# Performance work log

Hardware: AMD Instinct MI355X
Metric: run time of the kernel (lower is better)

## Reference

```python
import jax, jax.numpy as jnp
import numpy as np


def setup_inputs() -> dict:
    key = jax.random.key(0)
    ks = jax.random.split(key, 6)
    B, N, d = 8, 2048, 64
    h = jax.random.normal(ks[0], (B, N, d), dtype=jnp.float32)
    adj = jax.random.randint(ks[1], (B, N, N), 0, 2, dtype=jnp.int32)
    h_root = jax.random.normal(ks[2], (B, N), dtype=jnp.float32)
    weight = jax.random.normal(ks[3], (d, d), dtype=jnp.float32) * (1.0 / np.sqrt(d))
    a1 = jax.random.normal(ks[4], (d, 1), dtype=jnp.float32) * (1.0 / np.sqrt(d))
    a2 = jax.random.normal(ks[5], (d, 1), dtype=jnp.float32) * (1.0 / np.sqrt(d))
    return {"h": h, "adj": adj, "h_root": h_root, "weight": weight, "a1": a1, "a2": a2}


def reference(h, adj, h_root, weight, a1, a2):
    h0 = h
    hw = jax.nn.relu(jnp.matmul(h, weight))          # (B,N,d)
    t1 = jnp.matmul(hw, a1)                          # (B,N,1)
    t2 = jnp.matmul(hw, a2)                          # (B,N,1)
    # e[b,i,j] = relu(t1[b,i] + t2[b,j])  (broadcast, same as repeat/view in torch)
    e = jax.nn.relu(t1 + jnp.swapaxes(t2, -1, -2))   # (B,N,N)
    # FAITHFUL to source bug: pos0 = -9e15 * zeros_like(adj) == 0, so
    # non-edges get logit 0 (not -inf) before softmax.
    e = jnp.where(adj > 0, e, jnp.zeros_like(e))
    attention = jax.nn.softmax(e, axis=-1)           # (B,N,N)
    embedding = jnp.matmul(attention, hw)            # (B,N,d)
    # assign = h_root[:,:,None] @ ones(B,1,d) -> h_root broadcast over d;
    # assign > 0  <=>  h_root > 0 since ones are positive.
    assign = h_root[:, :, None] * jnp.ones((1, 1, hw.shape[-1]), dtype=hw.dtype)
    embedding = jnp.where(assign > 0, embedding, h0)
    return embedding
```

## Files before the change

kernel.cpp:

```cpp
#include <hip/hip_runtime.h>
#include <hip/hip_bf16.h>

#define BATCH 8
#define NN    2048
#define DD    64
#define BN    (BATCH * NN)
#define MWORDS 68

typedef __attribute__((ext_vector_type(8))) short bf16x8;
typedef __attribute__((ext_vector_type(4))) float f32x4;

static __device__ __forceinline__ unsigned f2bf_pk(float lo, float hi) {
  unsigned ul = __float_as_uint(lo);
  unsigned uh = __float_as_uint(hi);
  ul = (ul + 0x7fffu + ((ul >> 16) & 1u)) >> 16;
  uh = (uh + 0x7fffu + ((uh >> 16) & 1u)) & 0xffff0000u;
  return ul | uh;
}

__global__ __launch_bounds__(256) void kA(
    const float* __restrict__ h, const float* __restrict__ W,
    const float* __restrict__ a1, const float* __restrict__ a2,
    const int* __restrict__ adj, const float* __restrict__ h_root,
    unsigned short* __restrict__ hwT, float* __restrict__ t1,
    float* __restrict__ t2, unsigned* __restrict__ masks) {
  if (blockIdx.x >= 512) {
    const int row  = (blockIdx.x - 512) * 4 + (threadIdx.x >> 6);
    const int lane = threadIdx.x & 63;
    if (h_root[row] <= 0.f) return;
    const int* ap = adj + (size_t)row * NN + lane * 32;
    unsigned word = 0;
#pragma unroll
    for (int i = 0; i < 8; ++i) {
      int4 v = *reinterpret_cast<const int4*>(ap + i * 4);
      word |= (v.x > 0 ? 1u : 0u) << (i * 4 + 0);
      word |= (v.y > 0 ? 1u : 0u) << (i * 4 + 1);
      word |= (v.z > 0 ? 1u : 0u) << (i * 4 + 2);
      word |= (v.w > 0 ? 1u : 0u) << (i * 4 + 3);
    }
    masks[(size_t)row * 64 + lane] = word;
    return;
  }

  __shared__ float ht[64 * 36];
  __shared__ float Ws[64 * 64];
  __shared__ unsigned short bt[64 * 40];

  const int t  = threadIdx.x;
  const int r0 = blockIdx.x * 32;

#pragma unroll
  for (int r = 0; r < 4; ++r) {
    int f = t + 256 * r;
    reinterpret_cast<float4*>(Ws)[f] = reinterpret_cast<const float4*>(W)[f];
  }
#pragma unroll
  for (int r = 0; r < 2; ++r) {
    int f = t + 256 * r;
    int i = f >> 4, j4 = f & 15;
    float4 v = reinterpret_cast<const float4*>(h + (size_t)(r0 + i) * DD)[j4];
    ht[(4 * j4 + 0) * 36 + i] = v.x;
    ht[(4 * j4 + 1) * 36 + i] = v.y;
    ht[(4 * j4 + 2) * 36 + i] = v.z;
    ht[(4 * j4 + 3) * 36 + i] = v.w;
  }
  __syncthreads();

  const int trow = t >> 4, kcol = t & 15;
  float4 acc0 = make_float4(0.f, 0.f, 0.f, 0.f);
  float4 acc1 = make_float4(0.f, 0.f, 0.f, 0.f);

#pragma unroll 8
  for (int j = 0; j < 64; ++j) {
    float2 hv = *reinterpret_cast<const float2*>(&ht[j * 36 + 2 * trow]);
    float4 wv = reinterpret_cast<const float4*>(Ws)[j * 16 + kcol];
    acc0.x = fmaf(hv.x, wv.x, acc0.x); acc0.y = fmaf(hv.x, wv.y, acc0.y);
    acc0.z = fmaf(hv.x, wv.z, acc0.z); acc0.w = fmaf(hv.x, wv.w, acc0.w);
    acc1.x = fmaf(hv.y, wv.x, acc1.x); acc1.y = fmaf(hv.y, wv.y, acc1.y);
    acc1.z = fmaf(hv.y, wv.z, acc1.z); acc1.w = fmaf(hv.y, wv.w, acc1.w);
  }

  acc0.x = fmaxf(acc0.x, 0.f); acc0.y = fmaxf(acc0.y, 0.f);
  acc0.z = fmaxf(acc0.z, 0.f); acc0.w = fmaxf(acc0.w, 0.f);
  acc1.x = fmaxf(acc1.x, 0.f); acc1.y = fmaxf(acc1.y, 0.f);
  acc1.z = fmaxf(acc1.z, 0.f); acc1.w = fmaxf(acc1.w, 0.f);

  float4 a1v = reinterpret_cast<const float4*>(a1)[kcol];
  float4 a2v = reinterpret_cast<const float4*>(a2)[kcol];
  float s1_0 = acc0.x * a1v.x + acc0.y * a1v.y + acc0.z * a1v.z + acc0.w * a1v.w;
  float s1_1 = acc1.x * a1v.x + acc1.y * a1v.y + acc1.z * a1v.z + acc1.w * a1v.w;
  float s2_0 = acc0.x * a2v.x + acc0.y * a2v.y + acc0.z * a2v.z + acc0.w * a2v.w;
  float s2_1 = acc1.x * a2v.x + acc1.y * a2v.y + acc1.z * a2v.z + acc1.w * a2v.w;
#pragma unroll
  for (int mm = 1; mm <= 8; mm <<= 1) {
    s1_0 += __shfl_xor(s1_0, mm, 64);
    s1_1 += __shfl_xor(s1_1, mm, 64);
    s2_0 += __shfl_xor(s2_0, mm, 64);
    s2_1 += __shfl_xor(s2_1, mm, 64);
  }
  {
    int row = r0 + 2 * trow;
    if (kcol == 0) {
      t1[row] = s1_0; t1[row + 1] = s1_1;
      t2[row] = s2_0; t2[row + 1] = s2_1;
    }
  }

  {
    const float* a0 = &acc0.x;
    const float* a1p = &acc1.x;
#pragma unroll
    for (int c = 0; c < 4; ++c) {
      int k = 4 * kcol + c;
      *reinterpret_cast<unsigned*>(&bt[k * 40 + 2 * trow]) = f2bf_pk(a0[c], a1p[c]);
    }
  }
  __syncthreads();
  {
    int k = t >> 2, jp = t & 3;
    int g = k >> 4, n = k & 15;
    int bb = r0 >> 11;
    int jb = r0 & (NN - 1);
    int ks = jb >> 5;
    size_t base = ((((size_t)bb * (NN / 32) + ks) * 4 + g) * 64 + (jp * 16 + n)) * 8;
    *reinterpret_cast<int4*>(hwT + base) = *reinterpret_cast<const int4*>(&bt[k * 40 + jp * 8]);
  }
}

__global__ __launch_bounds__(256, 4) void k2_attn(
    const unsigned short* __restrict__ hwT, const unsigned* __restrict__ masks,
    const float* __restrict__ t1, const float* __restrict__ t2,
    const float* __restrict__ h, const float* __restrict__ h_root,
    float* __restrict__ out) {
  __shared__ unsigned maskS[16 * MWORDS];
  __shared__ float t2s[NN];
  __shared__ float os[4][16][68];
  __shared__ float denos[4][16];

  const int t    = threadIdx.x;
  const int b    = blockIdx.x & 7;
  const int i0   = (blockIdx.x >> 3) * 16;
  const int w    = t >> 6;
  const int lane = t & 63;
  const int m    = lane & 15;
  const int quad = lane >> 4;
  const int rowbase = b * NN + i0;

#pragma unroll
  for (int r = 0; r < 2; ++r)
    reinterpret_cast<float4*>(t2s)[t + 256 * r] =
        reinterpret_cast<const float4*>(t2 + b * NN)[t + 256 * r];

  {
    int row = t >> 4, w4 = t & 15;
    int4 mv = *reinterpret_cast<const int4*>(
        masks + ((size_t)(rowbase + row)) * 64 + w4 * 4);
    *reinterpret_cast<int4*>(&maskS[row * MWORDS + w4 * 4]) = mv;
  }
  __syncthreads();

  const float t1v = t1[rowbase + m];
  const int ks0 = w * 16;

  f32x4 acc[4];
#pragma unroll
  for (int g = 0; g < 4; ++g) acc[g] = (f32x4){0.f, 0.f, 0.f, 0.f};
  float den = 0.f;

  unsigned mcur = maskS[m * MWORDS + ks0];

#pragma unroll 1
  for (int kk = 0; kk < 16; ++kk) {
    const int ks = ks0 + kk;
    unsigned mnext = 0;
    if (kk + 1 < 16) mnext = maskS[m * MWORDS + ks + 1];

    const unsigned short* bp =
        hwT + ((((size_t)b * (NN / 32) + ks) * 4) * 64 + lane) * 8;
    bf16x8 B0 = *reinterpret_cast<const bf16x8*>(bp);
    bf16x8 B1 = *reinterpret_cast<const bf16x8*>(bp + 512);
    bf16x8 B2 = *reinterpret_cast<const bf16x8*>(bp + 1024);
    bf16x8 B3 = *reinterpret_cast<const bf16x8*>(bp + 1536);

    const float* t2p = &t2s[ks * 32 + quad * 8];
    float4 e0 = *reinterpret_cast<const float4*>(t2p);
    float4 e1 = *reinterpret_cast<const float4*>(t2p + 4);

    const unsigned mm8 = mcur >> (quad * 8);
    float p0 = (mm8 & 1u)   ? __expf(fmaxf(t1v + e0.x, 0.f)) : 1.f;
    float p1 = (mm8 & 2u)   ? __expf(fmaxf(t1v + e0.y, 0.f)) : 1.f;
    float p2 = (mm8 & 4u)   ? __expf(fmaxf(t1v + e0.z, 0.f)) : 1.f;
    float p3 = (mm8 & 8u)   ? __expf(fmaxf(t1v + e0.w, 0.f)) : 1.f;
    float p4 = (mm8 & 16u)  ? __expf(fmaxf(t1v + e1.x, 0.f)) : 1.f;
    float p5 = (mm8 & 32u)  ? __expf(fmaxf(t1v + e1.y, 0.f)) : 1.f;
    float p6 = (mm8 & 64u)  ? __expf(fmaxf(t1v + e1.z, 0.f)) : 1.f;
    float p7 = (mm8 & 128u) ? __expf(fmaxf(t1v + e1.w, 0.f)) : 1.f;
    den += ((p0 + p1) + (p2 + p3)) + ((p4 + p5) + (p6 + p7));

    union { bf16x8 v; unsigned u[4]; } Af;
    Af.u[0] = f2bf_pk(p0, p1); Af.u[1] = f2bf_pk(p2, p3);
    Af.u[2] = f2bf_pk(p4, p5); Af.u[3] = f2bf_pk(p6, p7);

    acc[0] = __builtin_amdgcn_mfma_f32_16x16x32_bf16(Af.v, B0, acc[0], 0, 0, 0);
    acc[1] = __builtin_amdgcn_mfma_f32_16x16x32_bf16(Af.v, B1, acc[1], 0, 0, 0);
    acc[2] = __builtin_amdgcn_mfma_f32_16x16x32_bf16(Af.v, B2, acc[2], 0, 0, 0);
    acc[3] = __builtin_amdgcn_mfma_f32_16x16x32_bf16(Af.v, B3, acc[3], 0, 0, 0);

    mcur = mnext;
  }

  den += __shfl_xor(den, 16, 64);
  den += __shfl_xor(den, 32, 64);
  if (quad == 0) denos[w][m] = den;

#pragma unroll
  for (int g = 0; g < 4; ++g)
#pragma unroll
    for (int r = 0; r < 4; ++r)
      os[w][quad * 4 + r][g * 16 + m] = acc[g][r];
  __syncthreads();

  {
    const int i = t >> 4, k4 = t & 15;
    float4 a = make_float4(0.f, 0.f, 0.f, 0.f);
    float d = 0.f;
#pragma unroll
    for (int ww = 0; ww < 4; ++ww) {
      float4 p = *reinterpret_cast<const float4*>(&os[ww][i][k4 * 4]);
      a.x += p.x; a.y += p.y; a.z += p.z; a.w += p.w;
      d += denos[ww][i];
    }
    const size_t row = (size_t)rowbase + i;
    float4 res;
    if (h_root[row] > 0.f) {
      const float inv = 1.f / d;
      res.x = a.x * inv; res.y = a.y * inv; res.z = a.z * inv; res.w = a.w * inv;
    } else {
      res = reinterpret_cast<const float4*>(h + row * DD)[k4];
    }
    reinterpret_cast<float4*>(out + row * DD)[k4] = res;
  }
}

extern "C" void kernel_launch(void* const* d_in, const int* in_sizes, int n_in,
                              void* d_out, int out_size, void* d_ws, size_t ws_size,
                              hipStream_t stream) {
  const float* h      = (const float*)d_in[0];
  const int*   adj    = (const int*)d_in[1];
  const float* h_root = (const float*)d_in[2];
  const float* W      = (const float*)d_in[3];
  const float* a1     = (const float*)d_in[4];
  const float* a2     = (const float*)d_in[5];
  float* out = (float*)d_out;

  unsigned short* hwT = (unsigned short*)d_ws;
  float* t1 = (float*)(hwT + (size_t)BN * DD);
  float* t2 = t1 + BN;
  unsigned* masks = (unsigned*)(t2 + BN);

  kA<<<512 + BN / 4, 256, 0, stream>>>(h, W, a1, a2, adj, h_root, hwT, t1, t2, masks);
  k2_attn<<<BATCH * (NN / 16), 256, 0, stream>>>(hwT, masks, t1, t2, h, h_root, out);
}
```

Baseline: 206.2 us.

## Process 32 rows per attention block and use hardware bf16 pack conversion

Each attention block now handles 32 query rows instead of 16, with two sets of MFMA accumulators sharing the same hwT B-fragments and t2 values. This halves B-operand global loads and t2 reads per row. The software bf16 rounding is replaced by the v_cvt_pk_bf16_f32 instruction to cut ALU work. Register pressure rises, so occupancy drops: launch bounds go to 2 and the grid halves.

```diff
diff --git a/kernel.cpp b/kernel.cpp
--- a/kernel.cpp
+++ b/kernel.cpp
@@ -16,6 +16,12 @@
   ul = (ul + 0x7fffu + ((ul >> 16) & 1u)) >> 16;
   uh = (uh + 0x7fffu + ((uh >> 16) & 1u)) & 0xffff0000u;
   return ul | uh;
+}
+
+static __device__ __forceinline__ unsigned cvtpk(float lo, float hi) {
+  unsigned r;
+  asm("v_cvt_pk_bf16_f32 %0, %1, %2" : "=v"(r) : "v"(lo), "v"(hi));
+  return r;
 }
 
 __global__ __launch_bounds__(256) void kA(
@@ -127,19 +133,19 @@
   }
 }
 
-__global__ __launch_bounds__(256, 4) void k2_attn(
+__global__ __launch_bounds__(256, 2) void k2_attn(
     const unsigned short* __restrict__ hwT, const unsigned* __restrict__ masks,
     const float* __restrict__ t1, const float* __restrict__ t2,
     const float* __restrict__ h, const float* __restrict__ h_root,
     float* __restrict__ out) {
-  __shared__ unsigned maskS[16 * MWORDS];
+  __shared__ unsigned maskS[32 * MWORDS];
   __shared__ float t2s[NN];
-  __shared__ float os[4][16][68];
-  __shared__ float denos[4][16];
+  __shared__ float os[4][32][68];
+  __shared__ float denos[4][32];
 
   const int t    = threadIdx.x;
   const int b    = blockIdx.x & 7;
-  const int i0   = (blockIdx.x >> 3) * 16;
+  const int i0   = (blockIdx.x >> 3) * 32;
   const int w    = t >> 6;
   const int lane = t & 63;
   const int m    = lane & 15;
@@ -151,29 +157,31 @@
     reinterpret_cast<float4*>(t2s)[t + 256 * r] =
         reinterpret_cast<const float4*>(t2 + b * NN)[t + 256 * r];
 
-  {
-    int row = t >> 4, w4 = t & 15;
+#pragma unroll
+  for (int r = 0; r < 2; ++r) {
+    int idx = t + 256 * r;
+    int row = idx >> 4, w4 = idx & 15;
     int4 mv = *reinterpret_cast<const int4*>(
         masks + ((size_t)(rowbase + row)) * 64 + w4 * 4);
     *reinterpret_cast<int4*>(&maskS[row * MWORDS + w4 * 4]) = mv;
   }
   __syncthreads();
 
-  const float t1v = t1[rowbase + m];
+  const float t1v0 = t1[rowbase + m];
+  const float t1v1 = t1[rowbase + 16 + m];
   const int ks0 = w * 16;
 
-  f32x4 acc[4];
-#pragma unroll
-  for (int g = 0; g < 4; ++g) acc[g] = (f32x4){0.f, 0.f, 0.f, 0.f};
-  float den = 0.f;
-
-  unsigned mcur = maskS[m * MWORDS + ks0];
-
-#pragma unroll 1
+  f32x4 acc[4][2];
+#pragma unroll
+  for (int g = 0; g < 4; ++g) {
+    acc[g][0] = (f32x4){0.f, 0.f, 0.f, 0.f};
+    acc[g][1] = (f32x4){0.f, 0.f, 0.f, 0.f};
+  }
+  float den0 = 0.f, den1 = 0.f;
+
+#pragma unroll 2
   for (int kk = 0; kk < 16; ++kk) {
     const int ks = ks0 + kk;
-    unsigned mnext = 0;
-    if (kk + 1 < 16) mnext = maskS[m * MWORDS + ks + 1];
 
     const unsigned short* bp =
         hwT + ((((size_t)b * (NN / 32) + ks) * 4) * 64 + lane) * 8;
@@ -186,42 +194,63 @@
     float4 e0 = *reinterpret_cast<const float4*>(t2p);
     float4 e1 = *reinterpret_cast<const float4*>(t2p + 4);
 
-    const unsigned mm8 = mcur >> (quad * 8);
-    float p0 = (mm8 & 1u)   ? __expf(fmaxf(t1v + e0.x, 0.f)) : 1.f;
-    float p1 = (mm8 & 2u)   ? __expf(fmaxf(t1v + e0.y, 0.f)) : 1.f;
-    float p2 = (mm8 & 4u)   ? __expf(fmaxf(t1v + e0.z, 0.f)) : 1.f;
-    float p3 = (mm8 & 8u)   ? __expf(fmaxf(t1v + e0.w, 0.f)) : 1.f;
-    float p4 = (mm8 & 16u)  ? __expf(fmaxf(t1v + e1.x, 0.f)) : 1.f;
-    float p5 = (mm8 & 32u)  ? __expf(fmaxf(t1v + e1.y, 0.f)) : 1.f;
-    float p6 = (mm8 & 64u)  ? __expf(fmaxf(t1v + e1.z, 0.f)) : 1.f;
-    float p7 = (mm8 & 128u) ? __expf(fmaxf(t1v + e1.w, 0.f)) : 1.f;
-    den += ((p0 + p1) + (p2 + p3)) + ((p4 + p5) + (p6 + p7));
-
-    union { bf16x8 v; unsigned u[4]; } Af;
-    Af.u[0] = f2bf_pk(p0, p1); Af.u[1] = f2bf_pk(p2, p3);
-    Af.u[2] = f2bf_pk(p4, p5); Af.u[3] = f2bf_pk(p6, p7);
-
-    acc[0] = __builtin_amdgcn_mfma_f32_16x16x32_bf16(Af.v, B0, acc[0], 0, 0, 0);
-    acc[1] = __builtin_amdgcn_mfma_f32_16x16x32_bf16(Af.v, B1, acc[1], 0, 0, 0);
-    acc[2] = __builtin_amdgcn_mfma_f32_16x16x32_bf16(Af.v, B2, acc[2], 0, 0, 0);
-    acc[3] = __builtin_amdgcn_mfma_f32_16x16x32_bf16(Af.v, B3, acc[3], 0, 0, 0);
-
-    mcur = mnext;
-  }
-
-  den += __shfl_xor(den, 16, 64);
-  den += __shfl_xor(den, 32, 64);
-  if (quad == 0) denos[w][m] = den;
+    const unsigned ma = maskS[m * MWORDS + ks] >> (quad * 8);
+    const unsigned mb = maskS[(m + 16) * MWORDS + ks] >> (quad * 8);
+
+    float p0 = (ma & 1u)   ? __expf(fmaxf(t1v0 + e0.x, 0.f)) : 1.f;
+    float p1 = (ma & 2u)   ? __expf(fmaxf(t1v0 + e0.y, 0.f)) : 1.f;
+    float p2 = (ma & 4u)   ? __expf(fmaxf(t1v0 + e0.z, 0.f)) : 1.f;
+    float p3 = (ma & 8u)   ? __expf(fmaxf(t1v0 + e0.w, 0.f)) : 1.f;
+    float p4 = (ma & 16u)  ? __expf(fmaxf(t1v0 + e1.x, 0.f)) : 1.f;
+    float p5 = (ma & 32u)  ? __expf(fmaxf(t1v0 + e1.y, 0.f)) : 1.f;
+    float p6 = (ma & 64u)  ? __expf(fmaxf(t1v0 + e1.z, 0.f)) : 1.f;
+    float p7 = (ma & 128u) ? __expf(fmaxf(t1v0 + e1.w, 0.f)) : 1.f;
+    den0 += ((p0 + p1) + (p2 + p3)) + ((p4 + p5) + (p6 + p7));
+
+    float q0 = (mb & 1u)   ? __expf(fmaxf(t1v1 + e0.x, 0.f)) : 1.f;
+    float q1 = (mb & 2u)   ? __expf(fmaxf(t1v1 + e0.y, 0.f)) : 1.f;
+    float q2 = (mb & 4u)   ? __expf(fmaxf(t1v1 + e0.z, 0.f)) : 1.f;
+    float q3 = (mb & 8u)   ? __expf(fmaxf(t1v1 + e0.w, 0.f)) : 1.f;
+    float q4 = (mb & 16u)  ? __expf(fmaxf(t1v1 + e1.x, 0.f)) : 1.f;
+    float q5 = (mb & 32u)  ? __expf(fmaxf(t1v1 + e1.y, 0.f)) : 1.f;
+    float q6 = (mb & 64u)  ? __expf(fmaxf(t1v1 + e1.z, 0.f)) : 1.f;
+    float q7 = (mb & 128u) ? __expf(fmaxf(t1v1 + e1.w, 0.f)) : 1.f;
+    den1 += ((q0 + q1) + (q2 + q3)) + ((q4 + q5) + (q6 + q7));
+
+    union { bf16x8 v; unsigned u[4]; } Af0, Af1;
+    Af0.u[0] = cvtpk(p0, p1); Af0.u[1] = cvtpk(p2, p3);
+    Af0.u[2] = cvtpk(p4, p5); Af0.u[3] = cvtpk(p6, p7);
+    Af1.u[0] = cvtpk(q0, q1); Af1.u[1] = cvtpk(q2, q3);
+    Af1.u[2] = cvtpk(q4, q5); Af1.u[3] = cvtpk(q6, q7);
+
+    acc[0][0] = __builtin_amdgcn_mfma_f32_16x16x32_bf16(Af0.v, B0, acc[0][0], 0, 0, 0);
+    acc[1][0] = __builtin_amdgcn_mfma_f32_16x16x32_bf16(Af0.v, B1, acc[1][0], 0, 0, 0);
+    acc[2][0] = __builtin_amdgcn_mfma_f32_16x16x32_bf16(Af0.v, B2, acc[2][0], 0, 0, 0);
+    acc[3][0] = __builtin_amdgcn_mfma_f32_16x16x32_bf16(Af0.v, B3, acc[3][0], 0, 0, 0);
+    acc[0][1] = __builtin_amdgcn_mfma_f32_16x16x32_bf16(Af1.v, B0, acc[0][1], 0, 0, 0);
+    acc[1][1] = __builtin_amdgcn_mfma_f32_16x16x32_bf16(Af1.v, B1, acc[1][1], 0, 0, 0);
+    acc[2][1] = __builtin_amdgcn_mfma_f32_16x16x32_bf16(Af1.v, B2, acc[2][1], 0, 0, 0);
+    acc[3][1] = __builtin_amdgcn_mfma_f32_16x16x32_bf16(Af1.v, B3, acc[3][1], 0, 0, 0);
+  }
+
+  den0 += __shfl_xor(den0, 16, 64);
+  den0 += __shfl_xor(den0, 32, 64);
+  den1 += __shfl_xor(den1, 16, 64);
+  den1 += __shfl_xor(den1, 32, 64);
+  if (quad == 0) { denos[w][m] = den0; denos[w][16 + m] = den1; }
 
 #pragma unroll
   for (int g = 0; g < 4; ++g)
 #pragma unroll
-    for (int r = 0; r < 4; ++r)
-      os[w][quad * 4 + r][g * 16 + m] = acc[g][r];
-  __syncthreads();
-
-  {
-    const int i = t >> 4, k4 = t & 15;
+    for (int r = 0; r < 4; ++r) {
+      os[w][quad * 4 + r][g * 16 + m]      = acc[g][0][r];
+      os[w][16 + quad * 4 + r][g * 16 + m] = acc[g][1][r];
+    }
+  __syncthreads();
+
+#pragma unroll
+  for (int rr = 0; rr < 2; ++rr) {
+    const int i = (t >> 4) + 16 * rr, k4 = t & 15;
     float4 a = make_float4(0.f, 0.f, 0.f, 0.f);
     float d = 0.f;
 #pragma unroll
@@ -259,5 +288,5 @@
   unsigned* masks = (unsigned*)(t2 + BN);
 
   kA<<<512 + BN / 4, 256, 0, stream>>>(h, W, a1, a2, adj, h_root, hwT, t1, t2, masks);
-  k2_attn<<<BATCH * (NN / 16), 256, 0, stream>>>(hwT, masks, t1, t2, h, h_root, out);
-}
+  k2_attn<<<BATCH * (NN / 32), 256, 0, stream>>>(hwT, masks, t1, t2, h, h_root, out);
+}
```

After: 204.5 us. About the same (-0.8%).
